# Performance work log

Hardware: AMD Instinct MI355X
Metric: run time of the kernel (lower is better)

Reference implementation:

```python
import jax, jax.numpy as jnp
import numpy as np

N = 50000        # nodes
E = 1_600_000    # edges
F = 32           # in/out channels
T = 4            # towers
FT = F // T      # per-tower channels = 8
ED = 16          # edge_dim
L = 5            # num PNA layers


def setup_inputs() -> dict:
    key = jax.random.key(0)
    ks = jax.random.split(key, 11)
    s = 0.2  # weight scale
    return {
        "x": jax.random.normal(ks[0], (N, F), jnp.float32),
        "edge_index": jax.random.randint(ks[1], (2, E), 0, N, dtype=jnp.int32),
        "edge_attr": jax.random.normal(ks[2], (E, ED), jnp.float32),
        # per-layer stacked PNAConv parameters
        "edge_W": jax.random.normal(ks[3], (L, ED, FT), jnp.float32) * s,
        "edge_b": jax.random.normal(ks[4], (L, FT), jnp.float32) * s,
        "pre_W": jax.random.normal(ks[5], (L, T, 3 * FT, FT), jnp.float32) * s,
        "pre_b": jax.random.normal(ks[6], (L, T, FT), jnp.float32) * s,
        "post_W": jax.random.normal(ks[7], (L, T, 4 * FT, FT), jnp.float32) * s,
        "post_b": jax.random.normal(ks[8], (L, T, FT), jnp.float32) * s,
        "lin_W": jax.random.normal(ks[9], (L, T * FT, F), jnp.float32) * s,
        "lin_b": jax.random.normal(ks[10], (L, F), jnp.float32) * s,
    }


def _pna_layer(x, src, dst, edge_attr, eW, eb, pW, pb, poW, pob, lW, lb):
    n = x.shape[0]
    xt = x.reshape(n, T, FT)                       # divide_input=True
    ee = edge_attr @ eW + eb                       # [E, FT], shared edge encoder
    xi = xt[dst]                                   # target node features [E, T, FT]
    xj = xt[src]                                   # source node features [E, T, FT]
    ee_b = jnp.broadcast_to(ee[:, None, :], (ee.shape[0], T, FT))
    h = jnp.concatenate([xi, xj, ee_b], axis=-1)   # [E, T, 3*FT]
    # per-tower pre-MLP (pre_layers=1)
    h = jnp.einsum('etk,tkf->etf', h, pW) + pb     # [E, T, FT]
    # aggregators: mean, sum, max (scaler = identity)
    ssum = jax.ops.segment_sum(h, dst, num_segments=n)
    cnt = jax.ops.segment_sum(jnp.ones((h.shape[0],), h.dtype), dst, num_segments=n)
    mean = ssum / jnp.maximum(cnt, 1.0)[:, None, None]
    mx = jax.ops.segment_max(h, dst, num_segments=n)
    mx = jnp.where(cnt[:, None, None] > 0, mx, 0.0)  # empty segments -> 0 (PyG convention)
    out = jnp.concatenate([xt, mean, ssum, mx], axis=-1)  # [N, T, 4*FT]
    # per-tower post-MLP (post_layers=1)
    out = jnp.einsum('ntk,tkf->ntf', out, poW) + pob      # [N, T, FT]
    out = out.reshape(n, T * FT) @ lW + lb                # final mixing linear
    return jax.nn.relu(out)


def reference(x, edge_index, edge_attr, edge_W, edge_b, pre_W, pre_b,
              post_W, post_b, lin_W, lin_b):
    src, dst = edge_index[0], edge_index[1]
    for l in range(L):
        x = _pna_layer(x, src, dst, edge_attr,
                       edge_W[l], edge_b[l], pre_W[l], pre_b[l],
                       post_W[l], post_b[l], lin_W[l], lin_b[l])
    return x
```

## Files before the change

kernel.cpp:

```cpp
#include <hip/hip_runtime.h>
#include <hip/hip_fp16.h>

#define NN 50000
#define NE 1600000
#define F 32
#define T 4
#define FT 8
#define ED 16
#define NLAYERS 5

typedef _Float16 h2 __attribute__((ext_vector_type(2)));

__device__ __forceinline__ float dot2(h2 a, h2 b, float c) {
#if __has_builtin(__builtin_amdgcn_fdot2)
    return __builtin_amdgcn_fdot2(a, b, c, false);
#else
    return c + (float)a.x * (float)b.x + (float)a.y * (float)b.y;
#endif
}


__global__ void zero_cnt(int* __restrict__ cnt) {
    int i = blockIdx.x * 256 + threadIdx.x;
    if (i < NN) cnt[i] = 0;
}

__global__ void count_kernel(const int* __restrict__ ei, int* __restrict__ cnt) {
    int e = blockIdx.x * 256 + threadIdx.x;
    if (e >= NE) return;
    atomicAdd(&cnt[ei[NE + e]], 1);
}

__global__ void scan_kernel(const int* __restrict__ cnt, int* __restrict__ row_ptr,
                            int* __restrict__ cursor) {
    __shared__ int wsum[16];
    __shared__ int carry_s;
    int tid = threadIdx.x;
    int lane = tid & 63, wid = tid >> 6;
    if (tid == 0) carry_s = 0;
    __syncthreads();
    for (int base = 0; base < NN; base += 1024) {
        int i = base + tid;
        int v = (i < NN) ? cnt[i] : 0;
        int s = v;
#pragma unroll
        for (int off = 1; off < 64; off <<= 1) {
            int tt = __shfl_up(s, off, 64);
            if (lane >= off) s += tt;
        }
        __syncthreads();
        if (lane == 63) wsum[wid] = s;
        __syncthreads();
        if (wid == 0 && lane < 16) {
            int w = wsum[lane];
            int ws = w;
#pragma unroll
            for (int off = 1; off < 16; off <<= 1) {
                int tt = __shfl_up(ws, off, 16);
                if (lane >= off) ws += tt;
            }
            wsum[lane] = ws - w;
        }
        __syncthreads();
        int excl = carry_s + wsum[wid] + s - v;
        if (i < NN) { row_ptr[i] = excl; cursor[i] = excl; }
        __syncthreads();
        if (tid == 1023) carry_s += wsum[15] + s;
    }
}

__global__ void build_kernel(const int* __restrict__ ei,
                             const float* __restrict__ eattr,
                             int* __restrict__ cursor,
                             int* __restrict__ src_s,
                             float4* __restrict__ eh) {
    int e = blockIdx.x * 256 + threadIdx.x;
    if (e >= NE) return;
    int src = ei[e];
    int dst = ei[NE + e];
    const float4* eap = (const float4*)(eattr + (size_t)e * ED);
    float4 v0 = eap[0], v1 = eap[1], v2 = eap[2], v3 = eap[3];
    union { __half hh[16]; float4 f4[2]; } u;
    u.hh[0]  = __float2half(v0.x); u.hh[1]  = __float2half(v0.y);
    u.hh[2]  = __float2half(v0.z); u.hh[3]  = __float2half(v0.w);
    u.hh[4]  = __float2half(v1.x); u.hh[5]  = __float2half(v1.y);
    u.hh[6]  = __float2half(v1.z); u.hh[7]  = __float2half(v1.w);
    u.hh[8]  = __float2half(v2.x); u.hh[9]  = __float2half(v2.y);
    u.hh[10] = __float2half(v2.z); u.hh[11] = __float2half(v2.w);
    u.hh[12] = __float2half(v3.x); u.hh[13] = __float2half(v3.y);
    u.hh[14] = __float2half(v3.z); u.hh[15] = __float2half(v3.w);
    int p = atomicAdd(&cursor[dst], 1);
    src_s[p] = src;
    eh[2 * (size_t)p]     = u.f4[0];
    eh[2 * (size_t)p + 1] = u.f4[1];
}

__global__ void layer_const(const float* __restrict__ edge_W,
                            const float* __restrict__ edge_b,
                            const float* __restrict__ pre_W,
                            const float* __restrict__ pre_b,
                            float4* __restrict__ wchp,
                            float* __restrict__ abias) {
    int idx = threadIdx.x;
    if (idx >= NLAYERS * 32) return;
    int l = idx >> 5, ch = idx & 31;
    int t = ch >> 3, f = ch & 7;
    const float* eW = edge_W + (size_t)l * ED * FT;
    const float* eb = edge_b + (size_t)l * FT;
    const float* pW = pre_W + (size_t)l * T * 24 * FT;
    const float* pb = pre_b + (size_t)l * T * FT;
    float pj[8];
#pragma unroll
    for (int j = 0; j < 8; j++) pj[j] = pW[(t * 24 + 16 + j) * 8 + f];
    union { _Float16 hh[16]; float4 f4[2]; } u;
#pragma unroll
    for (int k = 0; k < 16; k++) {
        float s = 0.f;
#pragma unroll
        for (int j = 0; j < 8; j++) s += eW[k * 8 + j] * pj[j];
        u.hh[k] = (_Float16)s;
    }
    float c0 = pb[t * 8 + f];
#pragma unroll
    for (int j = 0; j < 8; j++) c0 += eb[j] * pj[j];
    wchp[2 * idx]     = u.f4[0];
    wchp[2 * idx + 1] = u.f4[1];
    abias[idx] = c0;
}


__device__ __forceinline__ unsigned short f2bf_rne(float v) {
    unsigned u = __float_as_uint(v);
    return (unsigned short)((u + 0x7FFFu + ((u >> 16) & 1u)) >> 16);
}

__global__ void node_pre(const float* __restrict__ xin,
                         const float* __restrict__ preW,
                         unsigned short* __restrict__ b16) {
    int idx = blockIdx.x * 256 + threadIdx.x;
    if (idx >= NN * F) return;
    int n = idx >> 5, ch = idx & 31;
    int t = ch >> 3, f = ch & 7;
    const float* xrow = xin + n * F + t * FT;
    const float* wB = preW + (t * 24 + 8) * 8 + f;
    float bv = 0.f;
#pragma unroll
    for (int k = 0; k < 8; k++) bv += xrow[k] * wB[k * 8];
    b16[idx] = f2bf_rne(bv);
}

__global__ __launch_bounds__(256) void gather_post(
        const float* __restrict__ xin,
        const unsigned short* __restrict__ b16_in,
        unsigned short* __restrict__ b16_out,
        const float4* __restrict__ eh,
        const int* __restrict__ row_ptr, const int* __restrict__ cnt,
        const int* __restrict__ src_s,
        const float4* __restrict__ wchp_l,
        const float* __restrict__ abias_l,
        const float* __restrict__ preW,
        const float* __restrict__ postW, const float* __restrict__ postb,
        const float* __restrict__ linW, const float* __restrict__ linb,
        const float* __restrict__ preW_next,
        float* __restrict__ xout) {
    int tid = threadIdx.x;
    int wv = tid >> 6;
    int lane = tid & 63;
    int ch = lane & 31, half = lane >> 5;
    int n = blockIdx.x * 4 + wv;
    int t = ch >> 3, f = ch & 7;

    union { float4 f4[2]; h2 p[8]; } uw;
    uw.f4[0] = wchp_l[2 * ch];
    uw.f4[1] = wchp_l[2 * ch + 1];

    int rs = row_ptr[n], deg = cnt[n];
    int re = rs + deg;
    float S = 0.f, M = -3.4e38f;

#pragma unroll 4
    for (int i = rs + half; i < re; i += 2) {
        int s = src_s[i];
        float4 lo = eh[2 * (size_t)i];
        float4 hi = eh[2 * (size_t)i + 1];
        float h = __uint_as_float((unsigned)b16_in[s * F + ch] << 16);
        union { float4 f4; h2 p[4]; } ua, ub;
        ua.f4 = lo; ub.f4 = hi;
        h = dot2(ua.p[0], uw.p[0], h);
        h = dot2(ua.p[1], uw.p[1], h);
        h = dot2(ua.p[2], uw.p[2], h);
        h = dot2(ua.p[3], uw.p[3], h);
        h = dot2(ub.p[0], uw.p[4], h);
        h = dot2(ub.p[1], uw.p[5], h);
        h = dot2(ub.p[2], uw.p[6], h);
        h = dot2(ub.p[3], uw.p[7], h);
        S += h;
        M = fmaxf(M, h);
    }
    S += __shfl_xor(S, 32, 64);
    M = fmaxf(M, __shfl_xor(M, 32, 64));

    float xv = xin[(size_t)n * F + ch];
    float a_val = abias_l[ch];
#pragma unroll
    for (int j = 0; j < 8; j++)
        a_val += __shfl(xv, t * 8 + j, 64) * preW[(t * 24 + j) * 8 + f];

    float sum_h, mean_h, max_h;
    if (deg > 0) {
        sum_h = S + (float)deg * a_val;
        mean_h = sum_h / (float)deg;
        max_h = M + a_val;
    } else {
        sum_h = 0.f; mean_h = 0.f; max_h = 0.f;
    }

    float u2 = postb[t * 8 + f];
#pragma unroll
    for (int kk = 0; kk < 8; kk++) {
        int sl = t * 8 + kk;
        u2 += __shfl(xv,     sl, 64) * postW[(t * 32 + 0 * 8 + kk) * 8 + f];
        u2 += __shfl(mean_h, sl, 64) * postW[(t * 32 + 1 * 8 + kk) * 8 + f];
        u2 += __shfl(sum_h,  sl, 64) * postW[(t * 32 + 2 * 8 + kk) * 8 + f];
        u2 += __shfl(max_h,  sl, 64) * postW[(t * 32 + 3 * 8 + kk) * 8 + f];
    }
    float y = linb[ch];
#pragma unroll
    for (int k = 0; k < 32; k++)
        y += __shfl(u2, k, 64) * linW[k * 32 + ch];
    y = fmaxf(y, 0.f);
    if (half == 0)
        xout[(size_t)n * F + ch] = y;

    if (preW_next) {
        float bn = 0.f;
#pragma unroll
        for (int j = 0; j < 8; j++)
            bn += __shfl(y, t * 8 + j, 64) * preW_next[(t * 24 + 8 + j) * 8 + f];
        if (half == 0)
            b16_out[(size_t)n * F + ch] = f2bf_rne(bn);
    }
}


extern "C" void kernel_launch(void* const* d_in, const int* in_sizes, int n_in,
                              void* d_out, int out_size, void* d_ws, size_t ws_size,
                              hipStream_t stream) {
    const float* x      = (const float*)d_in[0];
    const int*   ei     = (const int*)d_in[1];
    const float* eattr  = (const float*)d_in[2];
    const float* edge_W = (const float*)d_in[3];
    const float* edge_b = (const float*)d_in[4];
    const float* pre_W  = (const float*)d_in[5];
    const float* pre_b  = (const float*)d_in[6];
    const float* post_W = (const float*)d_in[7];
    const float* post_b = (const float*)d_in[8];
    const float* lin_W  = (const float*)d_in[9];
    const float* lin_b  = (const float*)d_in[10];
    float* out = (float*)d_out;

    const size_t NC = (size_t)NN * F;
    char* p = (char*)d_ws;
    float4* eh    = (float4*)p;        p += sizeof(float4) * 2 * (size_t)NE;
    int* src_s    = (int*)p;           p += sizeof(int) * NE;
    int* cnt      = (int*)p;           p += sizeof(int) * NN;
    int* row_ptr  = (int*)p;           p += sizeof(int) * NN;
    int* cursor   = (int*)p;           p += sizeof(int) * NN;
    unsigned short* b16a = (unsigned short*)p;  p += sizeof(unsigned short) * NC;
    unsigned short* b16b = (unsigned short*)p;  p += sizeof(unsigned short) * NC;
    float* xb0    = (float*)p;         p += sizeof(float) * NC;
    float* xb1    = (float*)p;         p += sizeof(float) * NC;
    float4* wchp  = (float4*)p;        p += sizeof(float4) * 2 * NLAYERS * 32;
    float* abias  = (float*)p;         p += sizeof(float) * NLAYERS * 32;

    dim3 blk(256);
    int gN  = (NN + 255) / 256;
    int gE  = (NE + 255) / 256;
    int gNC = (NN * F + 255) / 256;
    int gG  = NN / 4;

    hipLaunchKernelGGL(zero_cnt,     dim3(gN), blk, 0, stream, cnt);
    hipLaunchKernelGGL(count_kernel, dim3(gE), blk, 0, stream, ei, cnt);
    hipLaunchKernelGGL(scan_kernel,  dim3(1), dim3(1024), 0, stream, cnt, row_ptr, cursor);
    hipLaunchKernelGGL(build_kernel, dim3(gE), blk, 0, stream, ei, eattr,
                       cursor, src_s, eh);
    hipLaunchKernelGGL(layer_const,  dim3(1), blk, 0, stream,
                       edge_W, edge_b, pre_W, pre_b, wchp, abias);

    hipLaunchKernelGGL(node_pre, dim3(gNC), blk, 0, stream, x, pre_W, b16a);

    const float* xin = x;
    for (int l = 0; l < NLAYERS; l++) {
        const float* pW  = pre_W  + (size_t)l * T * 24 * FT;
        const float* poW = post_W + (size_t)l * T * 32 * FT;
        const float* pob = post_b + (size_t)l * T * FT;
        const float* lW  = lin_W  + (size_t)l * F * F;
        const float* lb  = lin_b  + (size_t)l * F;
        const float* pWn = (l + 1 < NLAYERS) ? (pre_W + (size_t)(l + 1) * T * 24 * FT)
                                             : nullptr;
        float* xout = (l == NLAYERS - 1) ? out : ((l & 1) ? xb1 : xb0);
        const unsigned short* bin  = (l & 1) ? b16b : b16a;
        unsigned short*       bout = (l & 1) ? b16a : b16b;

        hipLaunchKernelGGL(gather_post, dim3(gG), blk, 0, stream,
                           xin, bin, pWn ? bout : nullptr, eh, row_ptr, cnt, src_s,
                           wchp + (size_t)l * 64, abias + (size_t)l * 32,
                           pW, poW, pob, lW, lb, pWn, xout);
        xin = xout;
    }
}
```

Baseline: 768.2 us.

## Split edge compute into separate kernel with padded quad-wise partial reductions

Pads each node's CSR segment to a multiple of four and adds an edge_compute kernel that evaluates four edges per thread-group per 4 channels, writing packed bf16 partial sum/max per quad. gather_post then only reduces these quad partials instead of gathering source features and doing dot products per edge. The goal is better load parallelism and vectorized gathers decoupled from per-node imbalance, at the cost of an extra kernel launch per layer, a large intermediate buffer write/read, and bf16 rounding of partial sums. It also splits the post/lin accumulation chains into four independent accumulators for ILP.

```diff
diff --git a/kernel.cpp b/kernel.cpp
--- a/kernel.cpp
+++ b/kernel.cpp
@@ -3,6 +3,8 @@
 
 #define NN 50000
 #define NE 1600000
+#define NEP4 (NE + 3 * NN)
+#define NQUAD (NEP4 / 4)
 #define F 32
 #define T 4
 #define FT 8
@@ -41,7 +43,7 @@
     __syncthreads();
     for (int base = 0; base < NN; base += 1024) {
         int i = base + tid;
-        int v = (i < NN) ? cnt[i] : 0;
+        int v = (i < NN) ? ((cnt[i] + 3) & ~3) : 0;
         int s = v;
 #pragma unroll
         for (int off = 1; off < 64; off <<= 1) {
@@ -67,6 +69,11 @@
         __syncthreads();
         if (tid == 1023) carry_s += wsum[15] + s;
     }
+}
+
+__global__ void init_src(int* __restrict__ src_s) {
+    int i = blockIdx.x * 256 + threadIdx.x;
+    if (i < NEP4) src_s[i] = -1;
 }
 
 __global__ void build_kernel(const int* __restrict__ ei,
@@ -90,7 +97,7 @@
     u.hh[12] = __float2half(v3.x); u.hh[13] = __float2half(v3.y);
     u.hh[14] = __float2half(v3.z); u.hh[15] = __float2half(v3.w);
     int p = atomicAdd(&cursor[dst], 1);
-    src_s[p] = src;
+    src_s[p] = src << 5;
     eh[2 * (size_t)p]     = u.f4[0];
     eh[2 * (size_t)p + 1] = u.f4[1];
 }
@@ -149,14 +156,70 @@
     b16[idx] = f2bf_rne(bv);
 }
 
+__global__ __launch_bounds__(256) void edge_compute(
+        const unsigned short* __restrict__ b16,
+        const float4* __restrict__ eh,
+        const int* __restrict__ src_s,
+        const float4* __restrict__ wchp_l,
+        uint4* __restrict__ hp) {
+    int idx = blockIdx.x * 256 + threadIdx.x;
+    if (idx >= NQUAD * 8) return;
+    int q = idx >> 3, g = idx & 7;
+    int ch0 = g << 2;
+    size_t sb = (size_t)q * 4;
+
+    int s0 = src_s[sb + 0];
+    int s1 = src_s[sb + 1];
+    int s2 = src_s[sb + 2];
+    int s3 = src_s[sb + 3];
+    union { float4 f4[2]; h2 p[8]; } e0, e1, e2, e3;
+    e0.f4[0] = eh[2 * sb + 0]; e0.f4[1] = eh[2 * sb + 1];
+    e1.f4[0] = eh[2 * sb + 2]; e1.f4[1] = eh[2 * sb + 3];
+    e2.f4[0] = eh[2 * sb + 4]; e2.f4[1] = eh[2 * sb + 5];
+    e3.f4[0] = eh[2 * sb + 6]; e3.f4[1] = eh[2 * sb + 7];
+    ushort4 b0 = *(const ushort4*)(b16 + (s0 < 0 ? 0 : s0) + ch0);
+    ushort4 b1 = *(const ushort4*)(b16 + (s1 < 0 ? 0 : s1) + ch0);
+    ushort4 b2 = *(const ushort4*)(b16 + (s2 < 0 ? 0 : s2) + ch0);
+    ushort4 b3 = *(const ushort4*)(b16 + (s3 < 0 ? 0 : s3) + ch0);
+    unsigned short ba[4] = {b0.x, b0.y, b0.z, b0.w};
+    unsigned short bb[4] = {b1.x, b1.y, b1.z, b1.w};
+    unsigned short bc[4] = {b2.x, b2.y, b2.z, b2.w};
+    unsigned short bd[4] = {b3.x, b3.y, b3.z, b3.w};
+
+    unsigned outv[4];
+#pragma unroll
+    for (int c = 0; c < 4; c++) {
+        union { float4 f4[2]; h2 p[8]; } wc;
+        wc.f4[0] = wchp_l[2 * (ch0 + c)];
+        wc.f4[1] = wchp_l[2 * (ch0 + c) + 1];
+        float h0 = __uint_as_float((unsigned)ba[c] << 16);
+        float h1 = __uint_as_float((unsigned)bb[c] << 16);
+        float h2v = __uint_as_float((unsigned)bc[c] << 16);
+        float h3 = __uint_as_float((unsigned)bd[c] << 16);
+#pragma unroll
+        for (int qq = 0; qq < 8; qq++) {
+            h0 = dot2(e0.p[qq], wc.p[qq], h0);
+            h1 = dot2(e1.p[qq], wc.p[qq], h1);
+            h2v = dot2(e2.p[qq], wc.p[qq], h2v);
+            h3 = dot2(e3.p[qq], wc.p[qq], h3);
+        }
+        float ssum = (s0 >= 0 ? h0 : 0.f) + (s1 >= 0 ? h1 : 0.f)
+                   + (s2 >= 0 ? h2v : 0.f) + (s3 >= 0 ? h3 : 0.f);
+        float smax = fmaxf(fmaxf(s0 >= 0 ? h0 : -3.4e38f, s1 >= 0 ? h1 : -3.4e38f),
+                           fmaxf(s2 >= 0 ? h2v : -3.4e38f, s3 >= 0 ? h3 : -3.4e38f));
+        unsigned lo = f2bf_rne(ssum);
+        unsigned hi = f2bf_rne(smax);
+        outv[c] = lo | (hi << 16);
+    }
+    uint4 o; o.x = outv[0]; o.y = outv[1]; o.z = outv[2]; o.w = outv[3];
+    hp[(size_t)q * 8 + g] = o;
+}
+
 __global__ __launch_bounds__(256) void gather_post(
         const float* __restrict__ xin,
-        const unsigned short* __restrict__ b16_in,
         unsigned short* __restrict__ b16_out,
-        const float4* __restrict__ eh,
+        const unsigned* __restrict__ hp,
         const int* __restrict__ row_ptr, const int* __restrict__ cnt,
-        const int* __restrict__ src_s,
-        const float4* __restrict__ wchp_l,
         const float* __restrict__ abias_l,
         const float* __restrict__ preW,
         const float* __restrict__ postW, const float* __restrict__ postb,
@@ -170,32 +233,17 @@
     int n = blockIdx.x * 4 + wv;
     int t = ch >> 3, f = ch & 7;
 
-    union { float4 f4[2]; h2 p[8]; } uw;
-    uw.f4[0] = wchp_l[2 * ch];
-    uw.f4[1] = wchp_l[2 * ch + 1];
-
     int rs = row_ptr[n], deg = cnt[n];
-    int re = rs + deg;
+    int nq = (deg + 3) >> 2;
+    const unsigned* hq = hp + (size_t)(rs >> 2) * 32;
+
     float S = 0.f, M = -3.4e38f;
-
-#pragma unroll 4
-    for (int i = rs + half; i < re; i += 2) {
-        int s = src_s[i];
-        float4 lo = eh[2 * (size_t)i];
-        float4 hi = eh[2 * (size_t)i + 1];
-        float h = __uint_as_float((unsigned)b16_in[s * F + ch] << 16);
-        union { float4 f4; h2 p[4]; } ua, ub;
-        ua.f4 = lo; ub.f4 = hi;
-        h = dot2(ua.p[0], uw.p[0], h);
-        h = dot2(ua.p[1], uw.p[1], h);
-        h = dot2(ua.p[2], uw.p[2], h);
-        h = dot2(ua.p[3], uw.p[3], h);
-        h = dot2(ub.p[0], uw.p[4], h);
-        h = dot2(ub.p[1], uw.p[5], h);
-        h = dot2(ub.p[2], uw.p[6], h);
-        h = dot2(ub.p[3], uw.p[7], h);
-        S += h;
-        M = fmaxf(M, h);
+    for (int k = half; k < nq; k += 2) {
+        unsigned v = hq[(size_t)k * 32 + ch];
+        float sq = __uint_as_float(v << 16);
+        float mq = __uint_as_float(v & 0xFFFF0000u);
+        S += sq;
+        M = fmaxf(M, mq);
     }
     S += __shfl_xor(S, 32, 64);
     M = fmaxf(M, __shfl_xor(M, 32, 64));
@@ -215,19 +263,26 @@
         sum_h = 0.f; mean_h = 0.f; max_h = 0.f;
     }
 
-    float u2 = postb[t * 8 + f];
+    float ua0 = 0.f, ua1 = 0.f, ua2 = 0.f, ua3 = 0.f;
 #pragma unroll
     for (int kk = 0; kk < 8; kk++) {
         int sl = t * 8 + kk;
-        u2 += __shfl(xv,     sl, 64) * postW[(t * 32 + 0 * 8 + kk) * 8 + f];
-        u2 += __shfl(mean_h, sl, 64) * postW[(t * 32 + 1 * 8 + kk) * 8 + f];
-        u2 += __shfl(sum_h,  sl, 64) * postW[(t * 32 + 2 * 8 + kk) * 8 + f];
-        u2 += __shfl(max_h,  sl, 64) * postW[(t * 32 + 3 * 8 + kk) * 8 + f];
-    }
-    float y = linb[ch];
-#pragma unroll
-    for (int k = 0; k < 32; k++)
-        y += __shfl(u2, k, 64) * linW[k * 32 + ch];
+        ua0 += __shfl(xv,     sl, 64) * postW[(t * 32 + 0 * 8 + kk) * 8 + f];
+        ua1 += __shfl(mean_h, sl, 64) * postW[(t * 32 + 1 * 8 + kk) * 8 + f];
+        ua2 += __shfl(sum_h,  sl, 64) * postW[(t * 32 + 2 * 8 + kk) * 8 + f];
+        ua3 += __shfl(max_h,  sl, 64) * postW[(t * 32 + 3 * 8 + kk) * 8 + f];
+    }
+    float u2 = postb[t * 8 + f] + ((ua0 + ua1) + (ua2 + ua3));
+
+    float y0 = 0.f, y1 = 0.f, y2 = 0.f, y3 = 0.f;
+#pragma unroll
+    for (int k = 0; k < 8; k++) {
+        y0 += __shfl(u2, k,      64) * linW[k * 32 + ch];
+        y1 += __shfl(u2, 8 + k,  64) * linW[(8 + k) * 32 + ch];
+        y2 += __shfl(u2, 16 + k, 64) * linW[(16 + k) * 32 + ch];
+        y3 += __shfl(u2, 24 + k, 64) * linW[(24 + k) * 32 + ch];
+    }
+    float y = linb[ch] + ((y0 + y1) + (y2 + y3));
     y = fmaxf(y, 0.f);
     if (half == 0)
         xout[(size_t)n * F + ch] = y;
@@ -261,8 +316,9 @@
 
     const size_t NC = (size_t)NN * F;
     char* p = (char*)d_ws;
-    float4* eh    = (float4*)p;        p += sizeof(float4) * 2 * (size_t)NE;
-    int* src_s    = (int*)p;           p += sizeof(int) * NE;
+    float4* eh    = (float4*)p;        p += sizeof(float4) * 2 * (size_t)NEP4;
+    uint4* hp     = (uint4*)p;         p += sizeof(uint4) * 8 * (size_t)NQUAD;
+    int* src_s    = (int*)p;           p += sizeof(int) * NEP4;
     int* cnt      = (int*)p;           p += sizeof(int) * NN;
     int* row_ptr  = (int*)p;           p += sizeof(int) * NN;
     int* cursor   = (int*)p;           p += sizeof(int) * NN;
@@ -274,14 +330,17 @@
     float* abias  = (float*)p;         p += sizeof(float) * NLAYERS * 32;
 
     dim3 blk(256);
-    int gN  = (NN + 255) / 256;
-    int gE  = (NE + 255) / 256;
-    int gNC = (NN * F + 255) / 256;
-    int gG  = NN / 4;
+    int gN   = (NN + 255) / 256;
+    int gE   = (NE + 255) / 256;
+    int gEP  = (NEP4 + 255) / 256;
+    int gNC  = (NN * F + 255) / 256;
+    int gEC  = (NQUAD * 8 + 255) / 256;
+    int gG   = NN / 4;
 
     hipLaunchKernelGGL(zero_cnt,     dim3(gN), blk, 0, stream, cnt);
     hipLaunchKernelGGL(count_kernel, dim3(gE), blk, 0, stream, ei, cnt);
     hipLaunchKernelGGL(scan_kernel,  dim3(1), dim3(1024), 0, stream, cnt, row_ptr, cursor);
+    hipLaunchKernelGGL(init_src,     dim3(gEP), blk, 0, stream, src_s);
     hipLaunchKernelGGL(build_kernel, dim3(gE), blk, 0, stream, ei, eattr,
                        cursor, src_s, eh);
     hipLaunchKernelGGL(layer_const,  dim3(1), blk, 0, stream,
@@ -302,9 +361,11 @@
         const unsigned short* bin  = (l & 1) ? b16b : b16a;
         unsigned short*       bout = (l & 1) ? b16a : b16b;
 
+        hipLaunchKernelGGL(edge_compute, dim3(gEC), blk, 0, stream,
+                           bin, eh, src_s, wchp + (size_t)l * 64, hp);
         hipLaunchKernelGGL(gather_post, dim3(gG), blk, 0, stream,
-                           xin, bin, pWn ? bout : nullptr, eh, row_ptr, cnt, src_s,
-                           wchp + (size_t)l * 64, abias + (size_t)l * 32,
+                           xin, pWn ? bout : nullptr, (const unsigned*)hp,
+                           row_ptr, cnt, abias + (size_t)l * 32,
                            pW, poW, pob, lW, lb, pWn, xout);
         xin = xout;
     }
```

Result: slower. 875.1 us (+13.9%).

## Assign one block per node with eight edge groups and LDS reduction

Applied to the files above, without the earlier changes.

The gather kernel now gives each node a whole 256-thread block: eight 32-lane groups walk the node's edges with stride 8 and combine their partial sum and max through shared memory. Only the first wave then runs the post-MLP and mixing linear, which now use split accumulators to shorten dependency chains. Source indices are stored pre-multiplied by 32 so the gather skips a multiply. The goal is more memory-level parallelism per node, at the cost of a barrier, three idle waves during the epilogue, and 50000 launched blocks.

```diff
diff --git a/kernel.cpp b/kernel.cpp
--- a/kernel.cpp
+++ b/kernel.cpp
@@ -90,7 +90,7 @@
     u.hh[12] = __float2half(v3.x); u.hh[13] = __float2half(v3.y);
     u.hh[14] = __float2half(v3.z); u.hh[15] = __float2half(v3.w);
     int p = atomicAdd(&cursor[dst], 1);
-    src_s[p] = src;
+    src_s[p] = src << 5;
     eh[2 * (size_t)p]     = u.f4[0];
     eh[2 * (size_t)p + 1] = u.f4[1];
 }
@@ -163,11 +163,11 @@
         const float* __restrict__ linW, const float* __restrict__ linb,
         const float* __restrict__ preW_next,
         float* __restrict__ xout) {
+    __shared__ float2 part[8][32];
     int tid = threadIdx.x;
-    int wv = tid >> 6;
-    int lane = tid & 63;
-    int ch = lane & 31, half = lane >> 5;
-    int n = blockIdx.x * 4 + wv;
+    int g = tid >> 5;
+    int ch = tid & 31;
+    int n = blockIdx.x;
     int t = ch >> 3, f = ch & 7;
 
     union { float4 f4[2]; h2 p[8]; } uw;
@@ -176,14 +176,13 @@
 
     int rs = row_ptr[n], deg = cnt[n];
     int re = rs + deg;
+
     float S = 0.f, M = -3.4e38f;
-
-#pragma unroll 4
-    for (int i = rs + half; i < re; i += 2) {
+    for (int i = rs + g; i < re; i += 8) {
         int s = src_s[i];
         float4 lo = eh[2 * (size_t)i];
         float4 hi = eh[2 * (size_t)i + 1];
-        float h = __uint_as_float((unsigned)b16_in[s * F + ch] << 16);
+        float h = __uint_as_float((unsigned)b16_in[s + ch] << 16);
         union { float4 f4; h2 p[4]; } ua, ub;
         ua.f4 = lo; ub.f4 = hi;
         h = dot2(ua.p[0], uw.p[0], h);
@@ -197,8 +196,18 @@
         S += h;
         M = fmaxf(M, h);
     }
-    S += __shfl_xor(S, 32, 64);
-    M = fmaxf(M, __shfl_xor(M, 32, 64));
+    part[g][ch] = make_float2(S, M);
+    __syncthreads();
+    if (tid >= 64) return;
+
+    int half = tid >> 5;
+    S = 0.f; M = -3.4e38f;
+#pragma unroll
+    for (int k = 0; k < 8; k++) {
+        float2 pm = part[k][ch];
+        S += pm.x;
+        M = fmaxf(M, pm.y);
+    }
 
     float xv = xin[(size_t)n * F + ch];
     float a_val = abias_l[ch];
@@ -215,19 +224,26 @@
         sum_h = 0.f; mean_h = 0.f; max_h = 0.f;
     }
 
-    float u2 = postb[t * 8 + f];
+    float ua0 = 0.f, ua1 = 0.f, ua2 = 0.f, ua3 = 0.f;
 #pragma unroll
     for (int kk = 0; kk < 8; kk++) {
         int sl = t * 8 + kk;
-        u2 += __shfl(xv,     sl, 64) * postW[(t * 32 + 0 * 8 + kk) * 8 + f];
-        u2 += __shfl(mean_h, sl, 64) * postW[(t * 32 + 1 * 8 + kk) * 8 + f];
-        u2 += __shfl(sum_h,  sl, 64) * postW[(t * 32 + 2 * 8 + kk) * 8 + f];
-        u2 += __shfl(max_h,  sl, 64) * postW[(t * 32 + 3 * 8 + kk) * 8 + f];
-    }
-    float y = linb[ch];
-#pragma unroll
-    for (int k = 0; k < 32; k++)
-        y += __shfl(u2, k, 64) * linW[k * 32 + ch];
+        ua0 += __shfl(xv,     sl, 64) * postW[(t * 32 + 0 * 8 + kk) * 8 + f];
+        ua1 += __shfl(mean_h, sl, 64) * postW[(t * 32 + 1 * 8 + kk) * 8 + f];
+        ua2 += __shfl(sum_h,  sl, 64) * postW[(t * 32 + 2 * 8 + kk) * 8 + f];
+        ua3 += __shfl(max_h,  sl, 64) * postW[(t * 32 + 3 * 8 + kk) * 8 + f];
+    }
+    float u2 = postb[t * 8 + f] + ((ua0 + ua1) + (ua2 + ua3));
+
+    float y0 = 0.f, y1 = 0.f, y2 = 0.f, y3 = 0.f;
+#pragma unroll
+    for (int k = 0; k < 8; k++) {
+        y0 += __shfl(u2, k,      64) * linW[k * 32 + ch];
+        y1 += __shfl(u2, 8 + k,  64) * linW[(8 + k) * 32 + ch];
+        y2 += __shfl(u2, 16 + k, 64) * linW[(16 + k) * 32 + ch];
+        y3 += __shfl(u2, 24 + k, 64) * linW[(24 + k) * 32 + ch];
+    }
+    float y = linb[ch] + ((y0 + y1) + (y2 + y3));
     y = fmaxf(y, 0.f);
     if (half == 0)
         xout[(size_t)n * F + ch] = y;
@@ -277,7 +293,6 @@
     int gN  = (NN + 255) / 256;
     int gE  = (NE + 255) / 256;
     int gNC = (NN * F + 255) / 256;
-    int gG  = NN / 4;
 
     hipLaunchKernelGGL(zero_cnt,     dim3(gN), blk, 0, stream, cnt);
     hipLaunchKernelGGL(count_kernel, dim3(gE), blk, 0, stream, ei, cnt);
@@ -302,7 +317,7 @@
         const unsigned short* bin  = (l & 1) ? b16b : b16a;
         unsigned short*       bout = (l & 1) ? b16a : b16b;
 
-        hipLaunchKernelGGL(gather_post, dim3(gG), blk, 0, stream,
+        hipLaunchKernelGGL(gather_post, dim3(NN), blk, 0, stream,
                            xin, bin, pWn ? bout : nullptr, eh, row_ptr, cnt, src_s,
                            wchp + (size_t)l * 64, abias + (size_t)l * 32,
                            pW, poW, pob, lW, lb, pWn, xout);
```

New measurement: 869.5 us. 1.13x slower.
